# Kernel tuning notes

Hardware: AMD Instinct MI355X
Metric: run time of the kernel (lower is better)

The kernel has to match this reference:

```python
import jax, jax.numpy as jnp
import numpy as np

EPS = 1e-6

def _ln(x):
    # LayerNorm without affine, biased variance (matches torch default)
    m = jnp.mean(x, axis=-1, keepdims=True)
    v = jnp.var(x, axis=-1, keepdims=True)
    return (x - m) / jnp.sqrt(v + EPS)

def setup_inputs() -> dict:
    key = jax.random.key(0)
    ks = jax.random.split(key, 12)
    B, N, C = 8, 4096, 768
    H = C * 4
    s = 0.02
    return {
        "x":   jax.random.normal(ks[0], (B, N, C), dtype=jnp.float32),
        "Wq":  jax.random.normal(ks[1], (C, C), dtype=jnp.float32) * s,
        "bq":  jnp.zeros((C,), dtype=jnp.float32),
        "Wkv": jax.random.normal(ks[2], (C, 2 * C), dtype=jnp.float32) * s,
        "bkv": jnp.zeros((2 * C,), dtype=jnp.float32),
        "Wo":  jax.random.normal(ks[3], (C, C), dtype=jnp.float32) * s,
        "bo":  jnp.zeros((C,), dtype=jnp.float32),
        "W1":  jax.random.normal(ks[4], (C, H), dtype=jnp.float32) * s,
        "b1":  jnp.zeros((H,), dtype=jnp.float32),
        "W2":  jax.random.normal(ks[5], (H, C), dtype=jnp.float32) * s,
        "b2":  jnp.zeros((C,), dtype=jnp.float32),
    }

def reference(x, Wq, bq, Wkv, bkv, Wo, bo, W1, b1, W2, b2):
    B, N, C = x.shape
    h = 16
    d = C // h
    scale = d ** -0.5

    xn = _ln(x)                          # norm1 over full sequence
    past = xn[:, :-1, :]                 # [B, N-1, C]
    cur = xn[:, -1, :]                   # [B, C]

    q = (cur @ Wq + bq).reshape(B, h, 1, d)                 # [B,h,1,d]
    kv = past @ Wkv + bkv                                   # [B,N-1,2C]
    k, v = jnp.split(kv, 2, axis=-1)
    k = k.reshape(B, N - 1, h, d).transpose(0, 2, 1, 3)     # [B,h,N-1,d]
    v = v.reshape(B, N - 1, h, d).transpose(0, 2, 1, 3)

    sim = jnp.einsum('bhqd,bhkd->bhqk', q, k) * scale       # [B,h,1,N-1]
    attn = jax.nn.softmax(sim, axis=-1)
    out = jnp.einsum('bhqk,bhkd->bhqd', attn, v)            # [B,h,1,d]
    out = out.transpose(0, 2, 1, 3).reshape(B, C)           # [B,C]
    out = out @ Wo + bo

    last = x[:, -1, :] + out                                # attn residual
    mlp = jax.nn.gelu(_ln(last) @ W1 + b1, approximate=True) @ W2 + b2
    last = last + mlp                                       # mlp residual

    return x.at[:, -1, :].set(last)
```

## Files before the change

### kernel.cpp

```cpp
#include <hip/hip_runtime.h>

#define B_ 8
#define N_ 4096
#define C_ 768
#define NP_ 4095
#define H_ 16
#define D_ 48
#define HID_ 3072
#define SCALE 0.14433756729740643f

typedef unsigned short u16;
typedef unsigned int u32;
typedef __attribute__((ext_vector_type(4))) float f32x4;
typedef __attribute__((ext_vector_type(8))) short short8;

__device__ __forceinline__ u32 f2bf_bits(float f){
  union { float f; u32 i; } v; v.f = f;
  return (v.i + 0x7fffu + ((v.i >> 16) & 1u)) >> 16;
}
__device__ __forceinline__ u32 pack2(float a, float b){
  return f2bf_bits(a) | (f2bf_bits(b) << 16);
}
__device__ __forceinline__ float bf2f(u16 u){
  union { u32 i; float f; } v; v.i = ((u32)u) << 16; return v.f;
}
__device__ __forceinline__ float2 up2(u32 u){
  union { u32 i; float f; } lo, hi;
  lo.i = u << 16; hi.i = u & 0xffff0000u;
  return make_float2(lo.f, hi.f);
}

__global__ __launch_bounds__(256) void k_q(const float* __restrict__ x,
    const float* __restrict__ Wq, const float* __restrict__ bq,
    float* __restrict__ qv)
{
  int b = blockIdx.y, t = threadIdx.x;
  int j0 = blockIdx.x*32;
  __shared__ float xs[C_];
  __shared__ float red[32][9];
  __shared__ float redA[4], redB[4];
  const float* xr = x + ((size_t)b*N_ + NP_)*C_;
  float v0 = xr[t], v1 = xr[t+256], v2 = xr[t+512];
  float s = v0+v1+v2, q = v0*v0+v1*v1+v2*v2;
  #pragma unroll
  for (int off=32; off; off>>=1){ s += __shfl_xor(s,off); q += __shfl_xor(q,off); }
  int w = t>>6, l = t&63;
  if (l==0){ redA[w]=s; redB[w]=q; }
  __syncthreads();
  s = redA[0]+redA[1]+redA[2]+redA[3];
  q = redB[0]+redB[1]+redB[2]+redB[3];
  float mean = s*(1.f/C_), var = q*(1.f/C_) - mean*mean;
  float rstd = rsqrtf(var + 1e-6f);
  xs[t] = (v0-mean)*rstd; xs[t+256] = (v1-mean)*rstd; xs[t+512] = (v2-mean)*rstd;
  __syncthreads();
  int jl = t&31, part = t>>5;
  const float* wp = Wq + (size_t)(part*96)*C_ + j0 + jl;
  const float* xp = xs + part*96;
  float acc = 0.f;
  #pragma unroll 8
  for (int c=0;c<96;c++) acc += xp[c]*wp[(size_t)c*C_];
  red[jl][part] = acc;
  __syncthreads();
  if (part==0){
    float a = bq[j0+jl];
    #pragma unroll
    for (int p=0;p<8;p++) a += red[jl][p];
    qv[(size_t)b*C_ + j0 + jl] = a;
  }
}

__global__ __launch_bounds__(256) void k_qw(const float* __restrict__ qv,
    const float* __restrict__ Wkv, float* __restrict__ qWf)
{
  int b = blockIdx.y, t = threadIdx.x;
  int c0 = blockIdx.x*16;
  __shared__ float qs[C_];
  for (int u=t; u<C_; u+=256) qs[u] = qv[(size_t)b*C_+u];
  __syncthreads();
  int h = t&15, cl = t>>4;
  int c = c0 + cl;
  const float* wp = Wkv + (size_t)c*(2*C_) + h*D_;
  const float* qh = qs + h*D_;
  float acc = 0.f;
  #pragma unroll
  for (int d=0; d<D_; d++) acc += qh[d]*wp[d];
  qWf[((size_t)b*H_ + h)*C_ + c] = acc;
}

__global__ __launch_bounds__(512) void k_attn(const float* __restrict__ x,
    const float* __restrict__ qWf, float* __restrict__ outp,
    float* __restrict__ ctx, float* __restrict__ denom)
{
  int b = blockIdx.y;
  int tid = threadIdx.x;
  int w = tid>>6, l = tid&63;
  int kblk = blockIdx.x*64;
  __shared__ u32 xlds[64][388];
  __shared__ u32 qlds[16][388];
  __shared__ float walds[64][20];
  __shared__ float wexpl[64][20];
  __shared__ float2 stl[64];
  __shared__ float pt[16][17];
  __shared__ float qwsum[16], sumS[16];
  const size_t xb = (size_t)b*N_*C_;

  #pragma unroll
  for (int it=0; it<4; ++it){
    int r = it*16 + (tid>>5);
    int sub = tid & 31;
    int kt = kblk + r;
    const float4* rp = (const float4*)(x + xb + (size_t)kt*C_);
    float4* op = (float4*)(outp + xb + (size_t)kt*C_);
    float4 v[6];
    #pragma unroll
    for (int j=0;j<6;j++) v[j] = rp[sub + 32*j];
    float s=0.f, q=0.f;
    #pragma unroll
    for (int j=0;j<6;j++){
      op[sub + 32*j] = v[j];
      s += v[j].x+v[j].y+v[j].z+v[j].w;
      q += v[j].x*v[j].x + v[j].y*v[j].y + v[j].z*v[j].z + v[j].w*v[j].w;
      int ci = (sub + 32*j)*2;
      xlds[r][ci]   = pack2(v[j].x, v[j].y);
      xlds[r][ci+1] = pack2(v[j].z, v[j].w);
    }
    #pragma unroll
    for (int off=1; off<32; off<<=1){ s += __shfl_xor(s,off); q += __shfl_xor(q,off); }
    if (sub==0){
      float mean = s*(1.f/C_), var = q*(1.f/C_) - mean*mean;
      stl[r] = make_float2(mean, rsqrtf(var + 1e-6f));
    }
  }
  for (int idx=tid; idx<H_*384; idx+=512){
    int h = idx/384, cu = idx - h*384;
    const float* qp = qWf + ((size_t)b*H_ + h)*C_ + cu*2;
    qlds[h][cu] = pack2(qp[0], qp[1]);
  }
  __syncthreads();
  if (tid < 256){
    int th = tid>>4, tl = tid&15;
    float ps = 0.f;
    #pragma unroll
    for (int j=0;j<24;j++){ float2 p = up2(qlds[th][tl*24+j]); ps += p.x + p.y; }
    pt[th][tl] = ps;
  }
  __syncthreads();
  if (tid < 16){
    float s2 = 0.f;
    #pragma unroll
    for (int j=0;j<16;j++) s2 += pt[tid][j];
    qwsum[tid] = s2;
  }
  f32x4 acc = {0.f,0.f,0.f,0.f};
  if (w < 4){
    int arow = w*16 + (l&15);
    int ko = (l>>4)*4;
    #pragma unroll
    for (int s2=0;s2<24;s2++){
      union{uint4 u; short8 v;} A, Bf;
      A.u  = *(const uint4*)&xlds[arow][s2*16 + ko];
      Bf.u = *(const uint4*)&qlds[l&15][s2*16 + ko];
      acc = __builtin_amdgcn_mfma_f32_16x16x32_bf16(A.v, Bf.v, acc, 0,0,0);
    }
  }
  __syncthreads();
  if (w < 4){
    int hh = l&15, mb = (l>>4)*4;
    #pragma unroll
    for (int r=0;r<4;r++){
      int rr = w*16 + mb + r;
      int kt = kblk + rr;
      float2 ms = stl[rr];
      float simv = ms.y * (acc[r] - ms.x*qwsum[hh]);
      float wv = (kt < NP_) ? __expf(simv*SCALE) : 0.f;
      wexpl[rr][hh] = wv;
      walds[rr][hh] = wv * ms.y;
    }
  }
  __syncthreads();
  if (tid < 16){
    float ds = 0.f, ss = 0.f;
    for (int k=0;k<64;k++){ ds += wexpl[k][tid]; ss += walds[k][tid]*stl[k].x; }
    atomicAdd(denom + (size_t)b*H_ + tid, ds);
    sumS[tid] = ss;
  }
  __syncthreads();
  int c0 = w*96;
  int cA = c0 + l;
  int cB = c0 + 64 + (l & 31);
  float accA[H_], accB[H_];
  #pragma unroll
  for (int h=0;h<H_;h++){ accA[h]=0.f; accB[h]=0.f; }
  const u16* xl = (const u16*)xlds;
  for (int k=0;k<64;k++){
    float xA = bf2f(xl[k*776 + cA]);
    float xB = bf2f(xl[k*776 + cB]);
    const float4* wp4 = (const float4*)&walds[k][0];
    float4 w0 = wp4[0], w1 = wp4[1], w2 = wp4[2], w3 = wp4[3];
    accA[0]+=w0.x*xA; accA[1]+=w0.y*xA; accA[2]+=w0.z*xA; accA[3]+=w0.w*xA;
    accA[4]+=w1.x*xA; accA[5]+=w1.y*xA; accA[6]+=w1.z*xA; accA[7]+=w1.w*xA;
    accA[8]+=w2.x*xA; accA[9]+=w2.y*xA; accA[10]+=w2.z*xA; accA[11]+=w2.w*xA;
    accA[12]+=w3.x*xA; accA[13]+=w3.y*xA; accA[14]+=w3.z*xA; accA[15]+=w3.w*xA;
    accB[0]+=w0.x*xB; accB[1]+=w0.y*xB; accB[2]+=w0.z*xB; accB[3]+=w0.w*xB;
    accB[4]+=w1.x*xB; accB[5]+=w1.y*xB; accB[6]+=w1.z*xB; accB[7]+=w1.w*xB;
    accB[8]+=w2.x*xB; accB[9]+=w2.y*xB; accB[10]+=w2.z*xB; accB[11]+=w2.w*xB;
    accB[12]+=w3.x*xB; accB[13]+=w3.y*xB; accB[14]+=w3.z*xB; accB[15]+=w3.w*xB;
  }
  float* cb = ctx + (size_t)b*H_*C_;
  #pragma unroll
  for (int h=0;h<H_;h++) atomicAdd(cb + h*C_ + cA, accA[h] - sumS[h]);
  if (l < 32){
    #pragma unroll
    for (int h=0;h<H_;h++) atomicAdd(cb + h*C_ + cB, accB[h] - sumS[h]);
  }
}

__global__ __launch_bounds__(256) void k_v(const float* __restrict__ ctx,
    const float* __restrict__ denom, const float* __restrict__ Wkv,
    const float* __restrict__ bkv, float* __restrict__ oat)
{
  int b = blockIdx.y, t = threadIdx.x;
  int t0 = blockIdx.x*32;
  int h0 = t0/D_;
  int h1 = (t0+31)/D_; if (h1 > H_-1) h1 = H_-1;
  __shared__ float cn[2][C_];
  __shared__ float red[32][9];
  float inv0 = 1.f/denom[(size_t)b*H_+h0];
  float inv1 = 1.f/denom[(size_t)b*H_+h1];
  for (int u=t; u<C_; u+=256){
    cn[0][u] = ctx[((size_t)b*H_+h0)*C_+u]*inv0;
    cn[1][u] = ctx[((size_t)b*H_+h1)*C_+u]*inv1;
  }
  __syncthreads();
  int jl = t&31, part = t>>5;
  int tt = t0 + jl;
  int hi = (tt/D_) - h0;
  const float* wp = Wkv + (size_t)(part*96)*(2*C_) + C_ + tt;
  const float* cp = cn[hi] + part*96;
  float acc = 0.f;
  #pragma unroll 8
  for (int c=0;c<96;c++) acc += cp[c]*wp[(size_t)c*(2*C_)];
  red[jl][part] = acc;
  __syncthreads();
  if (part==0){
    float a = bkv[C_ + tt];
    #pragma unroll
    for (int p=0;p<8;p++) a += red[jl][p];
    oat[(size_t)b*C_ + tt] = a;
  }
}

__global__ __launch_bounds__(256) void k_o(const float* __restrict__ x,
    const float* __restrict__ oat, const float* __restrict__ Wo,
    const float* __restrict__ bo, float* __restrict__ lastb)
{
  int b = blockIdx.y, t = threadIdx.x;
  int t0 = blockIdx.x*32;
  __shared__ float xs[C_];
  __shared__ float red[32][9];
  for (int u=t; u<C_; u+=256) xs[u] = oat[(size_t)b*C_+u];
  __syncthreads();
  int jl = t&31, part = t>>5;
  int tt = t0 + jl;
  const float* wp = Wo + (size_t)(part*96)*C_ + tt;
  const float* xp = xs + part*96;
  float acc = 0.f;
  #pragma unroll 8
  for (int c=0;c<96;c++) acc += xp[c]*wp[(size_t)c*C_];
  red[jl][part] = acc;
  __syncthreads();
  if (part==0){
    float a = bo[tt];
    #pragma unroll
    for (int p=0;p<8;p++) a += red[jl][p];
    lastb[(size_t)b*C_ + tt] = x[((size_t)b*N_ + NP_)*C_ + tt] + a;
  }
}

__global__ __launch_bounds__(256) void k_mlp1(const float* __restrict__ lastb,
    const float* __restrict__ W1, const float* __restrict__ b1,
    float* __restrict__ hid)
{
  int t = threadIdx.x;
  int j0 = blockIdx.x*16;
  __shared__ float xs[B_][C_];
  __shared__ float red[16][16][8];
  {
    int bb = t>>5, sub = t&31;
    const float* xr = lastb + (size_t)bb*C_;
    float s=0.f, q=0.f;
    #pragma unroll
    for (int j=0;j<24;j++){ float v = xr[sub+32*j]; s += v; q += v*v; }
    #pragma unroll
    for (int off=1; off<32; off<<=1){ s += __shfl_xor(s,off); q += __shfl_xor(q,off); }
    float mean = s*(1.f/C_), var = q*(1.f/C_) - mean*mean;
    float rstd = rsqrtf(var + 1e-6f);
    #pragma unroll
    for (int j=0;j<24;j++){ xs[bb][sub+32*j] = (xr[sub+32*j]-mean)*rstd; }
  }
  __syncthreads();
  int jl = t&15, part = t>>4;
  const float* wp = W1 + (size_t)(part*48)*HID_ + j0 + jl;
  float acc[B_];
  #pragma unroll
  for (int bb=0;bb<B_;bb++) acc[bb]=0.f;
  for (int c=0;c<48;c++){
    float wv = wp[(size_t)c*HID_];
    int cc = part*48 + c;
    #pragma unroll
    for (int bb=0;bb<B_;bb++) acc[bb] += xs[bb][cc]*wv;
  }
  #pragma unroll
  for (int bb=0;bb<B_;bb++) red[jl][part][bb] = acc[bb];
  __syncthreads();
  if (t < 128){
    int jl2 = t&15, bb = t>>4;
    float a = b1[j0+jl2];
    #pragma unroll
    for (int p=0;p<16;p++) a += red[jl2][p][bb];
    float t3 = a + 0.044715f*a*a*a;
    float g = 0.5f*a*(1.f + tanhf(0.7978845608f*t3));
    hid[(size_t)bb*HID_ + j0 + jl2] = g;
  }
}

__global__ __launch_bounds__(256) void k_mlp2(const float* __restrict__ hid,
    const float* __restrict__ W2, const float* __restrict__ b2,
    const float* __restrict__ lastb, float* __restrict__ outp)
{
  int t = threadIdx.x;
  int c0 = blockIdx.x*8;
  __shared__ float red[8][32][8];
  int ccl = t&7, part = t>>3;
  const float* wp = W2 + (size_t)(part*96)*C_ + c0 + ccl;
  float acc[B_];
  #pragma unroll
  for (int bb=0;bb<B_;bb++) acc[bb]=0.f;
  for (int j=0;j<96;j++){
    float wv = wp[(size_t)j*C_];
    int jj = part*96 + j;
    #pragma unroll
    for (int bb=0;bb<B_;bb++) acc[bb] += hid[(size_t)bb*HID_ + jj]*wv;
  }
  #pragma unroll
  for (int bb=0;bb<B_;bb++) red[ccl][part][bb] = acc[bb];
  __syncthreads();
  if (t < 64){
    int cc2 = t&7, bb = t>>3;
    float a = 0.f;
    #pragma unroll
    for (int p=0;p<32;p++) a += red[cc2][p][bb];
    int cc = c0 + cc2;
    a += b2[cc] + lastb[(size_t)bb*C_ + cc];
    outp[((size_t)bb*N_ + NP_)*C_ + cc] = a;
  }
}

extern "C" void kernel_launch(void* const* d_in, const int* in_sizes, int n_in,
                              void* d_out, int out_size, void* d_ws, size_t ws_size,
                              hipStream_t stream)
{
  (void)in_sizes; (void)n_in; (void)out_size; (void)ws_size;
  const float* x   = (const float*)d_in[0];
  const float* Wq  = (const float*)d_in[1];
  const float* bq  = (const float*)d_in[2];
  const float* Wkv = (const float*)d_in[3];
  const float* bkv = (const float*)d_in[4];
  const float* Wo  = (const float*)d_in[5];
  const float* bo  = (const float*)d_in[6];
  const float* W1  = (const float*)d_in[7];
  const float* b1  = (const float*)d_in[8];
  const float* W2  = (const float*)d_in[9];
  const float* b2  = (const float*)d_in[10];
  float* outp = (float*)d_out;
  float* ws = (float*)d_ws;
  float* ctx    = ws;
  float* denom  = ctx + 98304;
  float* qv     = denom + 128;
  float* oat    = qv + 6144;
  float* lastb  = oat + 6144;
  float* hid    = lastb + 6144;
  float* qWf    = hid + 24576;

  hipMemsetAsync(ctx, 0, (size_t)(98304+128)*sizeof(float), stream);
  hipLaunchKernelGGL(k_q,    dim3(24,B_), dim3(256), 0, stream, x, Wq, bq, qv);
  hipLaunchKernelGGL(k_qw,   dim3(48,B_), dim3(256), 0, stream, qv, Wkv, qWf);
  hipLaunchKernelGGL(k_attn, dim3(64,B_), dim3(512), 0, stream, x, qWf, outp, ctx, denom);
  hipLaunchKernelGGL(k_v,    dim3(24,B_), dim3(256), 0, stream, ctx, denom, Wkv, bkv, oat);
  hipLaunchKernelGGL(k_o,    dim3(24,B_), dim3(256), 0, stream, x, oat, Wo, bo, lastb);
  hipLaunchKernelGGL(k_mlp1, dim3(192), dim3(256), 0, stream, lastb, W1, b1, hid);
  hipLaunchKernelGGL(k_mlp2, dim3(96), dim3(256), 0, stream, hid, W2, b2, lastb, outp);
}
```

Measured before the change: 123.3 us.

## Drop LDS staging in attention kernel; normalize x on the fly from global

The attention kernel no longer stages a bf16 copy of the 64 key rows and the q·Wk vectors in shared memory. It re-reads x from global (likely L2-resident) and normalizes per element for both the MFMA scores and the context accumulation, which removes the mean-correction terms (qwsum, sumS). q·Wk is now written as bf16 by k_qw and read straight from global as MFMA B fragments. The block shrinks to 256 threads, each covering three columns, which cuts LDS use and sync phases so more blocks can be resident. The cost is three extra global reads of x per tile, and normalized activations are rounded to bf16 before the MFMA.

```diff
diff --git a/kernel.cpp b/kernel.cpp
--- a/kernel.cpp
+++ b/kernel.cpp
@@ -18,16 +18,9 @@
   union { float f; u32 i; } v; v.f = f;
   return (v.i + 0x7fffu + ((v.i >> 16) & 1u)) >> 16;
 }
+__device__ __forceinline__ u16 f2bf(float f){ return (u16)f2bf_bits(f); }
 __device__ __forceinline__ u32 pack2(float a, float b){
   return f2bf_bits(a) | (f2bf_bits(b) << 16);
-}
-__device__ __forceinline__ float bf2f(u16 u){
-  union { u32 i; float f; } v; v.i = ((u32)u) << 16; return v.f;
-}
-__device__ __forceinline__ float2 up2(u32 u){
-  union { u32 i; float f; } lo, hi;
-  lo.i = u << 16; hi.i = u & 0xffff0000u;
-  return make_float2(lo.f, hi.f);
 }
 
 __global__ __launch_bounds__(256) void k_q(const float* __restrict__ x,
@@ -70,7 +63,7 @@
 }
 
 __global__ __launch_bounds__(256) void k_qw(const float* __restrict__ qv,
-    const float* __restrict__ Wkv, float* __restrict__ qWf)
+    const float* __restrict__ Wkv, u16* __restrict__ qWb)
 {
   int b = blockIdx.y, t = threadIdx.x;
   int c0 = blockIdx.x*16;
@@ -84,118 +77,91 @@
   float acc = 0.f;
   #pragma unroll
   for (int d=0; d<D_; d++) acc += qh[d]*wp[d];
-  qWf[((size_t)b*H_ + h)*C_ + c] = acc;
-}
-
-__global__ __launch_bounds__(512) void k_attn(const float* __restrict__ x,
-    const float* __restrict__ qWf, float* __restrict__ outp,
+  qWb[((size_t)b*H_ + h)*C_ + c] = f2bf(acc);
+}
+
+__global__ __launch_bounds__(256) void k_attn(const float* __restrict__ x,
+    const u16* __restrict__ qWb, float* __restrict__ outp,
     float* __restrict__ ctx, float* __restrict__ denom)
 {
   int b = blockIdx.y;
   int tid = threadIdx.x;
   int w = tid>>6, l = tid&63;
   int kblk = blockIdx.x*64;
-  __shared__ u32 xlds[64][388];
-  __shared__ u32 qlds[16][388];
-  __shared__ float walds[64][20];
-  __shared__ float wexpl[64][20];
+  __shared__ float wexp[64][20];
   __shared__ float2 stl[64];
-  __shared__ float pt[16][17];
-  __shared__ float qwsum[16], sumS[16];
   const size_t xb = (size_t)b*N_*C_;
 
-  #pragma unroll
-  for (int it=0; it<4; ++it){
-    int r = it*16 + (tid>>5);
-    int sub = tid & 31;
+  #pragma unroll 4
+  for (int it=0; it<16; ++it){
+    int r = it*4 + w;
     int kt = kblk + r;
     const float4* rp = (const float4*)(x + xb + (size_t)kt*C_);
     float4* op = (float4*)(outp + xb + (size_t)kt*C_);
-    float4 v[6];
-    #pragma unroll
-    for (int j=0;j<6;j++) v[j] = rp[sub + 32*j];
-    float s=0.f, q=0.f;
-    #pragma unroll
-    for (int j=0;j<6;j++){
-      op[sub + 32*j] = v[j];
-      s += v[j].x+v[j].y+v[j].z+v[j].w;
-      q += v[j].x*v[j].x + v[j].y*v[j].y + v[j].z*v[j].z + v[j].w*v[j].w;
-      int ci = (sub + 32*j)*2;
-      xlds[r][ci]   = pack2(v[j].x, v[j].y);
-      xlds[r][ci+1] = pack2(v[j].z, v[j].w);
-    }
-    #pragma unroll
-    for (int off=1; off<32; off<<=1){ s += __shfl_xor(s,off); q += __shfl_xor(q,off); }
-    if (sub==0){
+    float4 v0 = rp[l], v1 = rp[l+64], v2 = rp[l+128];
+    op[l] = v0; op[l+64] = v1; op[l+128] = v2;
+    float s = v0.x+v0.y+v0.z+v0.w + v1.x+v1.y+v1.z+v1.w + v2.x+v2.y+v2.z+v2.w;
+    float q = v0.x*v0.x+v0.y*v0.y+v0.z*v0.z+v0.w*v0.w
+            + v1.x*v1.x+v1.y*v1.y+v1.z*v1.z+v1.w*v1.w
+            + v2.x*v2.x+v2.y*v2.y+v2.z*v2.z+v2.w*v2.w;
+    #pragma unroll
+    for (int off=32; off; off>>=1){ s += __shfl_xor(s,off); q += __shfl_xor(q,off); }
+    if (l==0){
       float mean = s*(1.f/C_), var = q*(1.f/C_) - mean*mean;
       stl[r] = make_float2(mean, rsqrtf(var + 1e-6f));
     }
   }
-  for (int idx=tid; idx<H_*384; idx+=512){
-    int h = idx/384, cu = idx - h*384;
-    const float* qp = qWf + ((size_t)b*H_ + h)*C_ + cu*2;
-    qlds[h][cu] = pack2(qp[0], qp[1]);
-  }
-  __syncthreads();
-  if (tid < 256){
-    int th = tid>>4, tl = tid&15;
-    float ps = 0.f;
-    #pragma unroll
-    for (int j=0;j<24;j++){ float2 p = up2(qlds[th][tl*24+j]); ps += p.x + p.y; }
-    pt[th][tl] = ps;
-  }
-  __syncthreads();
-  if (tid < 16){
-    float s2 = 0.f;
-    #pragma unroll
-    for (int j=0;j<16;j++) s2 += pt[tid][j];
-    qwsum[tid] = s2;
-  }
-  f32x4 acc = {0.f,0.f,0.f,0.f};
-  if (w < 4){
+  __syncthreads();
+
+  {
     int arow = w*16 + (l&15);
-    int ko = (l>>4)*4;
-    #pragma unroll
+    float2 ms = stl[arow];
+    const float* ar = x + xb + (size_t)(kblk + arow)*C_ + (l>>4)*8;
+    const u16* br = qWb + ((size_t)b*H_ + (l&15))*C_ + (l>>4)*8;
+    f32x4 acc = {0.f,0.f,0.f,0.f};
+    #pragma unroll 6
     for (int s2=0;s2<24;s2++){
+      float4 g0 = *(const float4*)(ar + s2*32);
+      float4 g1 = *(const float4*)(ar + s2*32 + 4);
+      uint4 nv;
+      nv.x = pack2((g0.x-ms.x)*ms.y, (g0.y-ms.x)*ms.y);
+      nv.y = pack2((g0.z-ms.x)*ms.y, (g0.w-ms.x)*ms.y);
+      nv.z = pack2((g1.x-ms.x)*ms.y, (g1.y-ms.x)*ms.y);
+      nv.w = pack2((g1.z-ms.x)*ms.y, (g1.w-ms.x)*ms.y);
       union{uint4 u; short8 v;} A, Bf;
-      A.u  = *(const uint4*)&xlds[arow][s2*16 + ko];
-      Bf.u = *(const uint4*)&qlds[l&15][s2*16 + ko];
+      A.u = nv;
+      Bf.u = *(const uint4*)(br + s2*32);
       acc = __builtin_amdgcn_mfma_f32_16x16x32_bf16(A.v, Bf.v, acc, 0,0,0);
     }
-  }
-  __syncthreads();
-  if (w < 4){
     int hh = l&15, mb = (l>>4)*4;
     #pragma unroll
     for (int r=0;r<4;r++){
       int rr = w*16 + mb + r;
       int kt = kblk + rr;
-      float2 ms = stl[rr];
-      float simv = ms.y * (acc[r] - ms.x*qwsum[hh]);
-      float wv = (kt < NP_) ? __expf(simv*SCALE) : 0.f;
-      wexpl[rr][hh] = wv;
-      walds[rr][hh] = wv * ms.y;
+      wexp[rr][hh] = (kt < NP_) ? __expf(acc[r]*SCALE) : 0.f;
     }
   }
   __syncthreads();
+
   if (tid < 16){
-    float ds = 0.f, ss = 0.f;
-    for (int k=0;k<64;k++){ ds += wexpl[k][tid]; ss += walds[k][tid]*stl[k].x; }
+    float ds = 0.f;
+    #pragma unroll 8
+    for (int k=0;k<64;k++) ds += wexp[k][tid];
     atomicAdd(denom + (size_t)b*H_ + tid, ds);
-    sumS[tid] = ss;
-  }
-  __syncthreads();
-  int c0 = w*96;
-  int cA = c0 + l;
-  int cB = c0 + 64 + (l & 31);
-  float accA[H_], accB[H_];
-  #pragma unroll
-  for (int h=0;h<H_;h++){ accA[h]=0.f; accB[h]=0.f; }
-  const u16* xl = (const u16*)xlds;
+  }
+
+  int c0 = w*192;
+  float accA[H_], accB[H_], accC[H_];
+  #pragma unroll
+  for (int h=0;h<H_;h++){ accA[h]=0.f; accB[h]=0.f; accC[h]=0.f; }
   for (int k=0;k<64;k++){
-    float xA = bf2f(xl[k*776 + cA]);
-    float xB = bf2f(xl[k*776 + cB]);
-    const float4* wp4 = (const float4*)&walds[k][0];
+    int kt = kblk + k;
+    const float* xr = x + xb + (size_t)kt*C_ + c0;
+    float2 ms = stl[k];
+    float xA = (xr[l]     - ms.x)*ms.y;
+    float xB = (xr[l+64]  - ms.x)*ms.y;
+    float xC = (xr[l+128] - ms.x)*ms.y;
+    const float4* wp4 = (const float4*)&wexp[k][0];
     float4 w0 = wp4[0], w1 = wp4[1], w2 = wp4[2], w3 = wp4[3];
     accA[0]+=w0.x*xA; accA[1]+=w0.y*xA; accA[2]+=w0.z*xA; accA[3]+=w0.w*xA;
     accA[4]+=w1.x*xA; accA[5]+=w1.y*xA; accA[6]+=w1.z*xA; accA[7]+=w1.w*xA;
@@ -205,13 +171,17 @@
     accB[4]+=w1.x*xB; accB[5]+=w1.y*xB; accB[6]+=w1.z*xB; accB[7]+=w1.w*xB;
     accB[8]+=w2.x*xB; accB[9]+=w2.y*xB; accB[10]+=w2.z*xB; accB[11]+=w2.w*xB;
     accB[12]+=w3.x*xB; accB[13]+=w3.y*xB; accB[14]+=w3.z*xB; accB[15]+=w3.w*xB;
+    accC[0]+=w0.x*xC; accC[1]+=w0.y*xC; accC[2]+=w0.z*xC; accC[3]+=w0.w*xC;
+    accC[4]+=w1.x*xC; accC[5]+=w1.y*xC; accC[6]+=w1.z*xC; accC[7]+=w1.w*xC;
+    accC[8]+=w2.x*xC; accC[9]+=w2.y*xC; accC[10]+=w2.z*xC; accC[11]+=w2.w*xC;
+    accC[12]+=w3.x*xC; accC[13]+=w3.y*xC; accC[14]+=w3.z*xC; accC[15]+=w3.w*xC;
   }
   float* cb = ctx + (size_t)b*H_*C_;
   #pragma unroll
-  for (int h=0;h<H_;h++) atomicAdd(cb + h*C_ + cA, accA[h] - sumS[h]);
-  if (l < 32){
-    #pragma unroll
-    for (int h=0;h<H_;h++) atomicAdd(cb + h*C_ + cB, accB[h] - sumS[h]);
+  for (int h=0;h<H_;h++){
+    atomicAdd(cb + h*C_ + c0 + l,       accA[h]);
+    atomicAdd(cb + h*C_ + c0 + 64 + l,  accB[h]);
+    atomicAdd(cb + h*C_ + c0 + 128 + l, accC[h]);
   }
 }
 
@@ -380,12 +350,12 @@
   float* oat    = qv + 6144;
   float* lastb  = oat + 6144;
   float* hid    = lastb + 6144;
-  float* qWf    = hid + 24576;
+  u16*   qWb    = (u16*)(hid + 24576);
 
   hipMemsetAsync(ctx, 0, (size_t)(98304+128)*sizeof(float), stream);
   hipLaunchKernelGGL(k_q,    dim3(24,B_), dim3(256), 0, stream, x, Wq, bq, qv);
-  hipLaunchKernelGGL(k_qw,   dim3(48,B_), dim3(256), 0, stream, qv, Wkv, qWf);
-  hipLaunchKernelGGL(k_attn, dim3(64,B_), dim3(512), 0, stream, x, qWf, outp, ctx, denom);
+  hipLaunchKernelGGL(k_qw,   dim3(48,B_), dim3(256), 0, stream, qv, Wkv, qWb);
+  hipLaunchKernelGGL(k_attn, dim3(64,B_), dim3(256), 0, stream, x, qWb, outp, ctx, denom);
   hipLaunchKernelGGL(k_v,    dim3(24,B_), dim3(256), 0, stream, ctx, denom, Wkv, bkv, oat);
   hipLaunchKernelGGL(k_o,    dim3(24,B_), dim3(256), 0, stream, x, oat, Wo, bo, lastb);
   hipLaunchKernelGGL(k_mlp1, dim3(192), dim3(256), 0, stream, lastb, W1, b1, hid);
```

Result: slower. 131.1 us (+6.3%).
